# Kernel tuning notes

Measured on AMD Instinct MI355X. Metric: run time of the kernel, lower is better.

The kernel has to match this reference:

```python
import jax, jax.numpy as jnp
import numpy as np
import math

EPS = 1e-5
L2_EPS = 1e-12  # torch F.normalize default eps


def _bitlinear(x, W):
    """BitNet b1.58-style BitLinear: ternary weights (per-tensor mean-abs scale)
    and per-token int8 absmax activation quantization. No bias.
    x: [..., in], W: [out, in] -> [..., out]
    """
    w_scale = jnp.clip(jnp.mean(jnp.abs(W)), EPS, None)
    W_q = jnp.clip(jnp.round(W / w_scale), -1.0, 1.0) * w_scale
    x_scale = 127.0 / jnp.clip(jnp.max(jnp.abs(x), axis=-1, keepdims=True), EPS, None)
    x_q = jnp.clip(jnp.round(x * x_scale), -128.0, 127.0) / x_scale
    return jnp.einsum('bsi,oi->bso', x_q, W_q)


def setup_inputs() -> dict:
    key = jax.random.key(0)
    k1, k2, k3 = jax.random.split(key, 3)
    B, S, D_in, P, D_out = 4, 4096, 2048, 16, 2048
    x = jax.random.normal(k1, (B, S, D_in), dtype=jnp.float32)
    # xavier_normal_: std = sqrt(2 / (fan_in + fan_out))
    Wk = jax.random.normal(k2, (P, D_in), dtype=jnp.float32) * math.sqrt(2.0 / (D_in + P))
    Wv = jax.random.normal(k3, (D_out, P), dtype=jnp.float32) * math.sqrt(2.0 / (P + D_out))
    return {"x": x, "Wk": Wk, "Wv": Wv}


def reference(x, Wk, Wv):
    # key projection -> [B, S, P]
    attn = _bitlinear(x, Wk)
    # gelu (exact erf form, torch default) + L2-normalize * sqrt(P)
    attn = jax.nn.gelu(attn, approximate=False)
    norm = jnp.clip(jnp.linalg.norm(attn, axis=-1, keepdims=True), L2_EPS, None)
    attn = attn / norm * jnp.sqrt(jnp.float32(attn.shape[-1]))
    # value projection -> [B, S, D_out]
    return _bitlinear(attn, Wv)
```

## Files before the change

### kernel.cpp

```cpp
#include <hip/hip_runtime.h>

#define DIN   2048
#define DOUT  2048
#define NP    16

#define HDR_OFF   0
#define WK4_OFF   256
#define WV4_OFF   (WK4_OFF + 32768)
#define XSW_OFF   (WV4_OFF + 32768)
#define XQ_OFF    (XSW_OFF + 65536)
#define Q2_OFF    (XQ_OFF + 33554432)
#define S2_OFF    (Q2_OFF + 262144)

static __device__ __forceinline__ int dot4(unsigned a, unsigned b, int c) {
#if defined(__has_builtin) && __has_builtin(__builtin_amdgcn_sdot4)
  return __builtin_amdgcn_sdot4((int)a, (int)b, c, false);
#else
  c += (int)(signed char)(a & 0xffu)        * (int)(signed char)(b & 0xffu);
  c += (int)(signed char)((a >> 8) & 0xffu) * (int)(signed char)((b >> 8) & 0xffu);
  c += (int)(signed char)((a >> 16) & 0xffu)* (int)(signed char)((b >> 16) & 0xffu);
  c += (int)(signed char)(a >> 24)          * (int)(signed char)(b >> 24);
  return c;
#endif
}

static __device__ __forceinline__ unsigned qmagic(float f, float xs) {
  return __float_as_uint(fmaf(f, xs, 12582912.0f)) & 0xffu;
}

static __device__ __forceinline__ unsigned q8(float f, float xs) {
  float t = f * xs;
  float r = rintf(t);
  r = fmaxf(-128.0f, fminf(127.0f, r));
  return ((unsigned)(int)r) & 0xffu;
}

__global__ __launch_bounds__(256) void k_prep(
    const float* __restrict__ Wk, const float* __restrict__ Wv,
    float* __restrict__ hdr, unsigned* __restrict__ wk4, unsigned* __restrict__ wv4)
{
  __shared__ float red[8][256];
  const int tid = threadIdx.x, b = blockIdx.x;
  const int isV = (b >= 32);
  const float4* W = (const float4*)(isV ? Wv : Wk);

  float4 own = make_float4(0.f, 0.f, 0.f, 0.f);
#pragma unroll
  for (int lb = 0; lb < 8; ++lb) {
    float s = 0.f;
#pragma unroll
    for (int i = 0; i < 4; ++i) {
      float4 v = W[lb * 1024 + i * 256 + tid];
      if (!isV && (lb * 4 + i) == b) own = v;
      s += fabsf(v.x) + fabsf(v.y) + fabsf(v.z) + fabsf(v.w);
    }
    red[lb][tid] = s;
  }
  __syncthreads();
#pragma unroll 1
  for (int o = 128; o > 0; o >>= 1) {
    if (tid < o) {
#pragma unroll
      for (int lb = 0; lb < 8; ++lb) red[lb][tid] += red[lb][tid + o];
    }
    __syncthreads();
  }
  float sum = 0.f;
#pragma unroll
  for (int lb = 0; lb < 8; ++lb) sum += red[lb][0];
  const float sc = fmaxf(sum * (1.0f / 32768.0f), 1e-5f);
  if (tid == 0 && (b == 0 || b == 32)) hdr[isV] = sc;

  if (!isV) {
    const int c = b * 256 + tid;
    unsigned pk = 0; const float* wp = &own.x;
#pragma unroll
    for (int j = 0; j < 4; ++j) {
      float r = rintf(wp[j] / sc);
      r = fmaxf(-1.0f, fminf(1.0f, r));
      pk |= (((unsigned)(int)r) & 0xffu) << (8 * j);
    }
    wk4[c] = pk;
  } else {
    const int o = (b - 32) * 256 + tid;
    unsigned u[4];
#pragma unroll
    for (int cc = 0; cc < 4; ++cc) {
      float4 w = ((const float4*)Wv)[o * 4 + cc];
      const float* wp = &w.x;
      unsigned pk = 0;
#pragma unroll
      for (int r = 0; r < 4; ++r) {
        float q = rintf(wp[r] / sc);
        q = fmaxf(-1.0f, fminf(1.0f, q));
        pk |= (((unsigned)(int)q) & 0xffu) << (8 * r);
      }
      u[cc] = pk;
    }
    const int m = o >> 8, r = o & 255, lr = r >> 2, j = r & 3;
    ((uint4*)wv4)[(m * 4 + j) * 64 + lr] = make_uint4(u[0], u[1], u[2], u[3]);
  }
}

__global__ __launch_bounds__(256) void k_quant(
    const float* __restrict__ x, unsigned* __restrict__ xqw,
    float* __restrict__ xsw)
{
  const int tid = threadIdx.x, l = tid & 63, wv = tid >> 6;
  const long tb = (long)blockIdx.x * 16 + wv * 4;
  const float4* xf = (const float4*)x;

#pragma unroll 1
  for (int i = 0; i < 4; ++i) {
    const long tok = tb + i;
    float4 a[8];
#pragma unroll
    for (int c = 0; c < 8; ++c) a[c] = xf[tok * 512 + c * 64 + l];

    float mx = 0.0f;
#pragma unroll
    for (int c = 0; c < 8; ++c) {
      mx = fmaxf(mx, fabsf(a[c].x)); mx = fmaxf(mx, fabsf(a[c].y));
      mx = fmaxf(mx, fabsf(a[c].z)); mx = fmaxf(mx, fabsf(a[c].w));
    }
#pragma unroll
    for (int d = 1; d < 64; d <<= 1) mx = fmaxf(mx, __shfl_xor(mx, d, 64));
    const float mcl = fmaxf(mx, 1e-5f);
    const float xs  = 127.0f / mcl;

#pragma unroll
    for (int c = 0; c < 8; ++c) {
      const unsigned q = qmagic(a[c].x, xs) | (qmagic(a[c].y, xs) << 8)
                       | (qmagic(a[c].z, xs) << 16) | (qmagic(a[c].w, xs) << 24);
      xqw[tok * 512 + c * 64 + l] = q;
    }
    if (l == 0) xsw[tok] = xs;
  }
}

__global__ __launch_bounds__(256) void k_mid(
    const unsigned* __restrict__ xq, const float* __restrict__ xsw,
    const unsigned* __restrict__ wk4, const float* __restrict__ hdr,
    uint4* __restrict__ q2w, float* __restrict__ s2w)
{
  __shared__ unsigned wkS[8192];
  __shared__ int accS[4][32][17];

  const int tid = threadIdx.x, l = tid & 63, wv = tid >> 6;
  const long t0 = (long)blockIdx.x * 32;

#pragma unroll 1
  for (int i = 0; i < 32; ++i) wkS[i * 256 + tid] = wk4[i * 256 + tid];
  __syncthreads();

  const int t = l >> 1, h = l & 1;
  const unsigned* xrow = xq + (t0 + t) * 512 + wv * 128 + h * 64;
  const unsigned* wbase = wkS + wv * 128 + h * 64;

  int acc[16];
#pragma unroll
  for (int p = 0; p < 16; ++p) acc[p] = 0;

#pragma unroll 2
  for (int c4 = 0; c4 < 16; ++c4) {
    const uint4 xv = *(const uint4*)(xrow + c4 * 4);
#pragma unroll
    for (int p = 0; p < 16; ++p) {
      const uint4 w = *(const uint4*)(wbase + p * 512 + c4 * 4);
      int d = acc[p];
      d = dot4(xv.x, w.x, d); d = dot4(xv.y, w.y, d);
      d = dot4(xv.z, w.z, d); d = dot4(xv.w, w.w, d);
      acc[p] = d;
    }
  }

#pragma unroll
  for (int p = 0; p < 16; ++p) acc[p] += __shfl_xor(acc[p], 1, 64);
  if (h == 0) {
#pragma unroll
    for (int p = 0; p < 16; ++p) accS[wv][t][p] = acc[p];
  }
  __syncthreads();

  if (tid < 32) {
    const long tok = t0 + tid;
    int r[16];
#pragma unroll
    for (int p = 0; p < 16; ++p)
      r[p] = ((accS[0][tid][p] + accS[1][tid][p]) + accS[2][tid][p]) + accS[3][tid][p];

    const float xs = xsw[tok];
    const float s1 = hdr[0] / xs;

    float g[16];
#pragma unroll
    for (int p = 0; p < 16; ++p) {
      const float fa = (float)r[p] * s1;
      g[p] = 0.5f * fa * (1.0f + erff(fa * 0.70710678118654752f));
    }
    float t1[8], t2[4], t3[2];
#pragma unroll
    for (int j = 0; j < 8; ++j) t1[j] = g[2 * j] * g[2 * j] + g[2 * j + 1] * g[2 * j + 1];
#pragma unroll
    for (int j = 0; j < 4; ++j) t2[j] = t1[2 * j] + t1[2 * j + 1];
    t3[0] = t2[0] + t2[1]; t3[1] = t2[2] + t2[3];
    const float ssum = t3[0] + t3[1];

    const float rn  = fmaxf(sqrtf(ssum), 1e-12f);
    const float inv = 4.0f / rn;
    float gn[16]; float am = 0.0f;
#pragma unroll
    for (int p = 0; p < 16; ++p) { gn[p] = g[p] * inv; am = fmaxf(am, fabsf(gn[p])); }
    const float mc2 = fmaxf(am, 1e-5f);
    const float xs2 = 127.0f / mc2;
    const float s2  = hdr[1] / xs2;

    unsigned w[4];
#pragma unroll
    for (int j = 0; j < 4; ++j)
      w[j] = q8(gn[4 * j], xs2)            | (q8(gn[4 * j + 1], xs2) << 8)
           | (q8(gn[4 * j + 2], xs2) << 16) | (q8(gn[4 * j + 3], xs2) << 24);
    q2w[tok] = make_uint4(w[0], w[1], w[2], w[3]);
    s2w[tok] = s2;
  }
}

__global__ __launch_bounds__(256) void k_out(
    const uint4* __restrict__ wv4t, const uint4* __restrict__ q2w,
    const float* __restrict__ s2w, float* __restrict__ out)
{
  const int tid = threadIdx.x, l = tid & 63, wv = tid >> 6;
  const int m = blockIdx.x & 7;
  const long tb = (long)(blockIdx.x >> 3) * 64 + wv * 16;

  const uint4 w0 = wv4t[(m * 4 + 0) * 64 + l];
  const uint4 w1 = wv4t[(m * 4 + 1) * 64 + l];
  const uint4 w2 = wv4t[(m * 4 + 2) * 64 + l];
  const uint4 w3 = wv4t[(m * 4 + 3) * 64 + l];

#pragma unroll 1
  for (int i = 0; i < 16; ++i) {
    const long tok = tb + i;
    const uint4 q  = q2w[tok];
    const float s2 = s2w[tok];
    int d; float h0, h1, h2, h3;
    d = dot4(q.x, w0.x, 0); d = dot4(q.y, w0.y, d);
    d = dot4(q.z, w0.z, d); d = dot4(q.w, w0.w, d); h0 = (float)d * s2;
    d = dot4(q.x, w1.x, 0); d = dot4(q.y, w1.y, d);
    d = dot4(q.z, w1.z, d); d = dot4(q.w, w1.w, d); h1 = (float)d * s2;
    d = dot4(q.x, w2.x, 0); d = dot4(q.y, w2.y, d);
    d = dot4(q.z, w2.z, d); d = dot4(q.w, w2.w, d); h2 = (float)d * s2;
    d = dot4(q.x, w3.x, 0); d = dot4(q.y, w3.y, d);
    d = dot4(q.z, w3.z, d); d = dot4(q.w, w3.w, d); h3 = (float)d * s2;
    *(float4*)(out + (size_t)tok * 2048 + m * 256 + l * 4) =
        make_float4(h0, h1, h2, h3);
  }
}

extern "C" void kernel_launch(void* const* d_in, const int* in_sizes, int n_in,
                              void* d_out, int out_size, void* d_ws, size_t ws_size,
                              hipStream_t stream) {
  const float* x  = (const float*)d_in[0];
  const float* Wk = (const float*)d_in[1];
  const float* Wv = (const float*)d_in[2];

  const int tokens = in_sizes[0] / DIN;

  char* ws = (char*)d_ws;
  float*    hdr = (float*)(ws + HDR_OFF);
  unsigned* wk4 = (unsigned*)(ws + WK4_OFF);
  unsigned* wv4 = (unsigned*)(ws + WV4_OFF);
  float*    xsw = (float*)(ws + XSW_OFF);
  unsigned* xqw = (unsigned*)(ws + XQ_OFF);
  uint4*    q2w = (uint4*)(ws + Q2_OFF);
  float*    s2w = (float*)(ws + S2_OFF);

  k_prep <<<40, 256, 0, stream>>>(Wk, Wv, hdr, wk4, wv4);
  k_quant<<<tokens / 16, 256, 0, stream>>>(x, xqw, xsw);
  k_mid  <<<tokens / 32, 256, 0, stream>>>(xqw, xsw, wk4, hdr, q2w, s2w);
  k_out  <<<(tokens / 64) * 8, 256, 0, stream>>>((const uint4*)wv4, q2w, s2w,
                                                 (float*)d_out);
}
```

Before: 274.1 us.

## Fuse activation quantization with key projection and GELU-normalize stage

Merges k_quant and k_mid into one kernel. Each wavefront quantizes two tokens into shared memory and computes the 16-wide key projection directly, with Wk repacked into a transposed layout so each lane streams one uint4 per step. GELU, the L2 norm and requantization now run across lanes with shuffles. This drops the 32 MB int8 intermediate write and its reread plus one kernel launch, at the cost of a more complex lane mapping. k_out's token loop is also unrolled by two.

Result: faster. 259.9 us (-5.2%).

```diff
diff --git a/kernel.cpp b/kernel.cpp
--- a/kernel.cpp
+++ b/kernel.cpp
@@ -5,11 +5,9 @@
 #define NP    16
 
 #define HDR_OFF   0
-#define WK4_OFF   256
-#define WV4_OFF   (WK4_OFF + 32768)
-#define XSW_OFF   (WV4_OFF + 32768)
-#define XQ_OFF    (XSW_OFF + 65536)
-#define Q2_OFF    (XQ_OFF + 33554432)
+#define WKT_OFF   256
+#define WVT_OFF   (WKT_OFF + 32768)
+#define Q2_OFF    (WVT_OFF + 32768)
 #define S2_OFF    (Q2_OFF + 262144)
 
 static __device__ __forceinline__ int dot4(unsigned a, unsigned b, int c) {
@@ -37,7 +35,7 @@
 
 __global__ __launch_bounds__(256) void k_prep(
     const float* __restrict__ Wk, const float* __restrict__ Wv,
-    float* __restrict__ hdr, unsigned* __restrict__ wk4, unsigned* __restrict__ wv4)
+    float* __restrict__ hdr, unsigned* __restrict__ wk4t, unsigned* __restrict__ wv4)
 {
   __shared__ float red[8][256];
   const int tid = threadIdx.x, b = blockIdx.x;
@@ -80,7 +78,9 @@
       r = fmaxf(-1.0f, fminf(1.0f, r));
       pk |= (((unsigned)(int)r) & 0xffu) << (8 * j);
     }
-    wk4[c] = pk;
+    const int p = c >> 9, kw = c & 511;
+    const int q = kw >> 7, c2 = (kw >> 2) & 31, sub = kw & 3;
+    wk4t[c2 * 256 + q * 64 + p * 4 + sub] = pk;
   } else {
     const int o = (b - 32) * 256 + tid;
     unsigned u[4];
@@ -102,17 +102,24 @@
   }
 }
 
-__global__ __launch_bounds__(256) void k_quant(
-    const float* __restrict__ x, unsigned* __restrict__ xqw,
-    float* __restrict__ xsw)
+__global__ __launch_bounds__(256) void kA2(
+    const float* __restrict__ x, const float* __restrict__ hdr,
+    const unsigned* __restrict__ wk4t, uint4* __restrict__ q2w,
+    float* __restrict__ s2w)
 {
   const int tid = threadIdx.x, l = tid & 63, wv = tid >> 6;
-  const long tb = (long)blockIdx.x * 16 + wv * 4;
-  const float4* xf = (const float4*)x;
-
-#pragma unroll 1
-  for (int i = 0; i < 4; ++i) {
-    const long tok = tb + i;
+  const long t0 = (long)blockIdx.x * 8 + wv * 2;
+
+  __shared__ unsigned xqs[4][2][544];
+
+  const float w1 = hdr[0], w2 = hdr[1];
+  const float4* xf  = (const float4*)x;
+  const uint4*  wkT = (const uint4*)wk4t;
+
+  float s1v[2];
+#pragma unroll
+  for (int tt = 0; tt < 2; ++tt) {
+    const long tok = t0 + tt;
     float4 a[8];
 #pragma unroll
     for (int c = 0; c < 8; ++c) a[c] = xf[tok * 512 + c * 64 + l];
@@ -127,101 +134,72 @@
     for (int d = 1; d < 64; d <<= 1) mx = fmaxf(mx, __shfl_xor(mx, d, 64));
     const float mcl = fmaxf(mx, 1e-5f);
     const float xs  = 127.0f / mcl;
+    s1v[tt] = w1 / xs;
 
 #pragma unroll
     for (int c = 0; c < 8; ++c) {
-      const unsigned q = qmagic(a[c].x, xs) | (qmagic(a[c].y, xs) << 8)
-                       | (qmagic(a[c].z, xs) << 16) | (qmagic(a[c].w, xs) << 24);
-      xqw[tok * 512 + c * 64 + l] = q;
-    }
-    if (l == 0) xsw[tok] = xs;
-  }
-}
-
-__global__ __launch_bounds__(256) void k_mid(
-    const unsigned* __restrict__ xq, const float* __restrict__ xsw,
-    const unsigned* __restrict__ wk4, const float* __restrict__ hdr,
-    uint4* __restrict__ q2w, float* __restrict__ s2w)
-{
-  __shared__ unsigned wkS[8192];
-  __shared__ int accS[4][32][17];
-
-  const int tid = threadIdx.x, l = tid & 63, wv = tid >> 6;
-  const long t0 = (long)blockIdx.x * 32;
-
-#pragma unroll 1
-  for (int i = 0; i < 32; ++i) wkS[i * 256 + tid] = wk4[i * 256 + tid];
-  __syncthreads();
-
-  const int t = l >> 1, h = l & 1;
-  const unsigned* xrow = xq + (t0 + t) * 512 + wv * 128 + h * 64;
-  const unsigned* wbase = wkS + wv * 128 + h * 64;
-
-  int acc[16];
-#pragma unroll
-  for (int p = 0; p < 16; ++p) acc[p] = 0;
-
-#pragma unroll 2
-  for (int c4 = 0; c4 < 16; ++c4) {
-    const uint4 xv = *(const uint4*)(xrow + c4 * 4);
-#pragma unroll
-    for (int p = 0; p < 16; ++p) {
-      const uint4 w = *(const uint4*)(wbase + p * 512 + c4 * 4);
-      int d = acc[p];
-      d = dot4(xv.x, w.x, d); d = dot4(xv.y, w.y, d);
-      d = dot4(xv.z, w.z, d); d = dot4(xv.w, w.w, d);
-      acc[p] = d;
-    }
-  }
-
-#pragma unroll
-  for (int p = 0; p < 16; ++p) acc[p] += __shfl_xor(acc[p], 1, 64);
-  if (h == 0) {
-#pragma unroll
-    for (int p = 0; p < 16; ++p) accS[wv][t][p] = acc[p];
-  }
-  __syncthreads();
-
-  if (tid < 32) {
-    const long tok = t0 + tid;
-    int r[16];
-#pragma unroll
-    for (int p = 0; p < 16; ++p)
-      r[p] = ((accS[0][tid][p] + accS[1][tid][p]) + accS[2][tid][p]) + accS[3][tid][p];
-
-    const float xs = xsw[tok];
-    const float s1 = hdr[0] / xs;
-
-    float g[16];
-#pragma unroll
-    for (int p = 0; p < 16; ++p) {
-      const float fa = (float)r[p] * s1;
-      g[p] = 0.5f * fa * (1.0f + erff(fa * 0.70710678118654752f));
-    }
-    float t1[8], t2[4], t3[2];
-#pragma unroll
-    for (int j = 0; j < 8; ++j) t1[j] = g[2 * j] * g[2 * j] + g[2 * j + 1] * g[2 * j + 1];
-#pragma unroll
-    for (int j = 0; j < 4; ++j) t2[j] = t1[2 * j] + t1[2 * j + 1];
-    t3[0] = t2[0] + t2[1]; t3[1] = t2[2] + t2[3];
-    const float ssum = t3[0] + t3[1];
-
-    const float rn  = fmaxf(sqrtf(ssum), 1e-12f);
-    const float inv = 4.0f / rn;
-    float gn[16]; float am = 0.0f;
-#pragma unroll
-    for (int p = 0; p < 16; ++p) { gn[p] = g[p] * inv; am = fmaxf(am, fabsf(gn[p])); }
+      const unsigned qv = qmagic(a[c].x, xs) | (qmagic(a[c].y, xs) << 8)
+                        | (qmagic(a[c].z, xs) << 16) | (qmagic(a[c].w, xs) << 24);
+      xqs[wv][tt][(c >> 1) * 136 + (c & 1) * 64 + l] = qv;
+    }
+  }
+
+  const unsigned* xb0 = &xqs[wv][0][(l >> 4) * 136];
+  const unsigned* xb1 = &xqs[wv][1][(l >> 4) * 136];
+  int ac0[4] = {0, 0, 0, 0}, ac1[4] = {0, 0, 0, 0};
+#pragma unroll
+  for (int c2 = 0; c2 < 32; ++c2) {
+    const uint4 w  = wkT[c2 * 64 + l];
+    const uint4 x0 = *(const uint4*)(xb0 + c2 * 4);
+    const uint4 x1 = *(const uint4*)(xb1 + c2 * 4);
+    int d0 = ac0[c2 & 3];
+    d0 = dot4(x0.x, w.x, d0); d0 = dot4(x0.y, w.y, d0);
+    d0 = dot4(x0.z, w.z, d0); d0 = dot4(x0.w, w.w, d0);
+    ac0[c2 & 3] = d0;
+    int d1 = ac1[c2 & 3];
+    d1 = dot4(x1.x, w.x, d1); d1 = dot4(x1.y, w.y, d1);
+    d1 = dot4(x1.z, w.z, d1); d1 = dot4(x1.w, w.w, d1);
+    ac1[c2 & 3] = d1;
+  }
+  int rrv[2];
+  rrv[0] = (ac0[0] + ac0[1]) + (ac0[2] + ac0[3]);
+  rrv[1] = (ac1[0] + ac1[1]) + (ac1[2] + ac1[3]);
+
+#pragma unroll
+  for (int tt = 0; tt < 2; ++tt) {
+    int rr = rrv[tt];
+    rr += __shfl_xor(rr, 16, 64);
+    rr += __shfl_xor(rr, 32, 64);
+
+    const float fa = (float)rr * s1v[tt];
+    const float gv = 0.5f * fa * (1.0f + erff(fa * 0.70710678118654752f));
+    float ss = gv * gv;
+    ss += __shfl_xor(ss, 1, 64); ss += __shfl_xor(ss, 2, 64);
+    ss += __shfl_xor(ss, 4, 64); ss += __shfl_xor(ss, 8, 64);
+    const float rn = fmaxf(sqrtf(ss), 1e-12f);
+    const float gn = gv * (4.0f / rn);
+    float am = fabsf(gn);
+    {
+      float o;
+      o = __shfl_xor(am, 1, 64); am = fmaxf(am, o);
+      o = __shfl_xor(am, 2, 64); am = fmaxf(am, o);
+      o = __shfl_xor(am, 4, 64); am = fmaxf(am, o);
+      o = __shfl_xor(am, 8, 64); am = fmaxf(am, o);
+    }
     const float mc2 = fmaxf(am, 1e-5f);
     const float xs2 = 127.0f / mc2;
-    const float s2  = hdr[1] / xs2;
-
-    unsigned w[4];
-#pragma unroll
-    for (int j = 0; j < 4; ++j)
-      w[j] = q8(gn[4 * j], xs2)            | (q8(gn[4 * j + 1], xs2) << 8)
-           | (q8(gn[4 * j + 2], xs2) << 16) | (q8(gn[4 * j + 3], xs2) << 24);
-    q2w[tok] = make_uint4(w[0], w[1], w[2], w[3]);
-    s2w[tok] = s2;
+    const float s2  = w2 / xs2;
+
+    unsigned sh = q8(gn, xs2) << ((l & 3) * 8);
+    sh |= (unsigned)__shfl_xor((int)sh, 1, 64);
+    sh |= (unsigned)__shfl_xor((int)sh, 2, 64);
+    const unsigned wa = (unsigned)__shfl_xor((int)sh, 4, 64);
+    const unsigned wb = (unsigned)__shfl_xor((int)sh, 8, 64);
+    const unsigned wc = (unsigned)__shfl_xor((int)sh, 12, 64);
+    if (l == 0) {
+      q2w[t0 + tt] = make_uint4(sh, wa, wb, wc);
+      s2w[t0 + tt] = s2;
+    }
   }
 }
 
@@ -238,7 +216,7 @@
   const uint4 w2 = wv4t[(m * 4 + 2) * 64 + l];
   const uint4 w3 = wv4t[(m * 4 + 3) * 64 + l];
 
-#pragma unroll 1
+#pragma unroll 2
   for (int i = 0; i < 16; ++i) {
     const long tok = tb + i;
     const uint4 q  = q2w[tok];
@@ -267,17 +245,14 @@
   const int tokens = in_sizes[0] / DIN;
 
   char* ws = (char*)d_ws;
-  float*    hdr = (float*)(ws + HDR_OFF);
-  unsigned* wk4 = (unsigned*)(ws + WK4_OFF);
-  unsigned* wv4 = (unsigned*)(ws + WV4_OFF);
-  float*    xsw = (float*)(ws + XSW_OFF);
-  unsigned* xqw = (unsigned*)(ws + XQ_OFF);
-  uint4*    q2w = (uint4*)(ws + Q2_OFF);
-  float*    s2w = (float*)(ws + S2_OFF);
-
-  k_prep <<<40, 256, 0, stream>>>(Wk, Wv, hdr, wk4, wv4);
-  k_quant<<<tokens / 16, 256, 0, stream>>>(x, xqw, xsw);
-  k_mid  <<<tokens / 32, 256, 0, stream>>>(xqw, xsw, wk4, hdr, q2w, s2w);
-  k_out  <<<(tokens / 64) * 8, 256, 0, stream>>>((const uint4*)wv4, q2w, s2w,
-                                                 (float*)d_out);
-}
+  float*    hdr  = (float*)(ws + HDR_OFF);
+  unsigned* wk4t = (unsigned*)(ws + WKT_OFF);
+  unsigned* wv4  = (unsigned*)(ws + WVT_OFF);
+  uint4*    q2w  = (uint4*)(ws + Q2_OFF);
+  float*    s2w  = (float*)(ws + S2_OFF);
+
+  k_prep<<<40, 256, 0, stream>>>(Wk, Wv, hdr, wk4t, wv4);
+  kA2   <<<tokens / 8, 256, 0, stream>>>(x, hdr, wk4t, q2w, s2w);
+  k_out <<<(tokens / 64) * 8, 256, 0, stream>>>((const uint4*)wv4, q2w, s2w,
+                                                (float*)d_out);
+}
```
